# Performance work log

Measured on AMD Instinct MI355X. Metric: run time of the kernel, lower is better.

Reference implementation:

```python
import jax, jax.numpy as jnp
import numpy as np

PRED_STEPS = 12
N_NEG = 100
TEMP = 0.1
EPS = 1e-12


def _l2norm(x):
    # matches torch F.normalize(dim=-1): x / max(||x||, eps)
    n = jnp.sqrt(jnp.sum(x * x, axis=-1, keepdims=True))
    return x / jnp.maximum(n, EPS)


def setup_inputs() -> dict:
    key = jax.random.key(0)
    k1, k2, k3, k4 = jax.random.split(key, 4)
    B, T, D = 8, 256, 256
    context = jax.random.normal(k1, (B, T, D), dtype=jnp.float32)
    targets = jax.random.normal(k2, (B, T, D), dtype=jnp.float32)
    W = jax.random.normal(k3, (PRED_STEPS, D, D), dtype=jnp.float32) * (1.0 / np.sqrt(D))
    b = jax.random.normal(k4, (PRED_STEPS, D), dtype=jnp.float32) * 0.01
    return {"context": context, "targets": targets, "W": W, "b": b}


def reference(context, targets, W, b):
    B, T, D = context.shape
    neg_key = jax.random.key(1234)
    total = jnp.zeros((), dtype=context.dtype)
    count = 0
    for step in range(1, PRED_STEPS + 1):
        if T - step <= 0:
            break
        T2 = T - step
        ctx = context[:, :T2, :]                        # (B,T2,D)
        pos = targets[:, step:, :]                      # (B,T2,D)
        # per-step linear predictor (torch Linear: x @ W^T + b)
        query = jnp.einsum('btd,ed->bte', ctx, W[step - 1]) + b[step - 1]
        query = _l2norm(query)
        pos_n = _l2norm(pos)                            # also serves as the negative pool
        pos_sim = jnp.sum(query * pos_n, axis=-1, keepdims=True) / TEMP  # (B,T2,1)
        # random in-batch negatives (deterministic per-step key)
        neg_idx = jax.random.randint(jax.random.fold_in(neg_key, step),
                                     (B, T2, N_NEG), 0, B * T2)
        flat = pos_n.reshape(B * T2, D)
        negs = flat[neg_idx]                            # (B,T2,K,D) gather
        neg_sim = jnp.einsum('btd,btkd->btk', query, negs) / TEMP  # (B,T2,K)
        logits = jnp.concatenate([pos_sim, neg_sim], axis=-1)      # (B,T2,1+K)
        # cross-entropy with label 0 == -log_softmax(logits)[..., 0], averaged
        loss_step = -jnp.mean(jax.nn.log_softmax(logits, axis=-1)[..., 0])
        total = total + loss_step
        count += 1
    return total / max(count, 1)
```

## Files before the change

kernel.cpp:

```cpp
#include <hip/hip_runtime.h>
#include <stdint.h>

#define BB 8
#define TT 256
#define DD 256
#define NSTEP 12
#define NNEG 100
#define NPART (255 * BB * NSTEP)

typedef _Float16 h2 __attribute__((ext_vector_type(2)));
typedef _Float16 f16x8 __attribute__((ext_vector_type(8)));
typedef float f32x4 __attribute__((ext_vector_type(4)));

#if __has_builtin(__builtin_amdgcn_fdot2)
__device__ __forceinline__ float fdot2(h2 a, h2 b, float c) {
  return __builtin_amdgcn_fdot2(a, b, c, false);
}
#else
__device__ __forceinline__ float fdot2(h2 a, h2 b, float c) {
  return c + (float)a.x * (float)b.x + (float)a.y * (float)b.y;
}
#endif

__device__ __forceinline__ h2 e5m2_lo(uint32_t w) {
#if __has_builtin(__builtin_amdgcn_perm)
  uint32_t r = __builtin_amdgcn_perm(0u, w, 0x010c000cu);
#else
  uint32_t r = ((w & 0xFFu) << 8) | ((w & 0xFF00u) << 16);
#endif
  union { uint32_t u; h2 h; } c; c.u = r; return c.h;
}
__device__ __forceinline__ h2 e5m2_hi(uint32_t w) {
#if __has_builtin(__builtin_amdgcn_perm)
  uint32_t r = __builtin_amdgcn_perm(0u, w, 0x030c020cu);
#else
  uint32_t r = ((w >> 8) & 0xFF00u) | ((w >> 16) & 0xFF000000u) | (((w >> 16) & 0xFFu) << 8);
#endif
  union { uint32_t u; h2 h; } c; c.u = r; return c.h;
}

__device__ __forceinline__ uint32_t f32_to_e5m2(float f) {
  union { _Float16 h; uint16_t u; } c; c.h = (_Float16)f;
  uint16_t h = c.u;
  return (uint32_t)((uint16_t)(h + (uint16_t)0x7F + (uint16_t)((h >> 8) & 1u)) >> 8) & 0xFFu;
}

__host__ __device__ __forceinline__ void tf2x32(uint32_t k0, uint32_t k1,
                                                uint32_t x0, uint32_t x1,
                                                uint32_t &y0, uint32_t &y1) {
  const uint32_t ks2 = k0 ^ k1 ^ 0x1BD11BDAu;
  x0 += k0; x1 += k1;
#define TF_R(r) { x0 += x1; x1 = (x1 << (r)) | (x1 >> (32 - (r))); x1 ^= x0; }
  TF_R(13) TF_R(15) TF_R(26) TF_R(6)
  x0 += k1; x1 += ks2 + 1u;
  TF_R(17) TF_R(29) TF_R(16) TF_R(24)
  x0 += ks2; x1 += k0 + 2u;
  TF_R(13) TF_R(15) TF_R(26) TF_R(6)
  x0 += k0; x1 += k1 + 3u;
  TF_R(17) TF_R(29) TF_R(16) TF_R(24)
  x0 += k1; x1 += ks2 + 4u;
  TF_R(13) TF_R(15) TF_R(26) TF_R(6)
  x0 += ks2; x1 += k0 + 5u;
#undef TF_R
  y0 = x0; y1 = x1;
}

struct IdxParams {
  uint32_t k1x[NSTEP], k1y[NSTEP], k2x[NSTEP], k2y[NSTEP];
  uint32_t mult[NSTEP];
  uint32_t Msp[NSTEP], Ssp[NSTEP], Asp[NSTEP];
  uint32_t Mt2[NSTEP], St2[NSTEP], At2[NSTEP];
};

static void magicu(uint32_t d, uint32_t* M, uint32_t* s, uint32_t* a) {
  uint32_t p, nc, delta, q1, r1, q2, r2;
  *a = 0;
  nc = 0xFFFFFFFFu - (0u - d) % d;
  p = 31;
  q1 = 0x80000000u / nc; r1 = 0x80000000u - q1 * nc;
  q2 = 0x7FFFFFFFu / d;  r2 = 0x7FFFFFFFu - q2 * d;
  do {
    p = p + 1;
    if (r1 >= nc - r1) { q1 = 2*q1 + 1; r1 = 2*r1 - nc; }
    else               { q1 = 2*q1;     r1 = 2*r1; }
    if (r2 + 1 >= d - r2) {
      if (q2 >= 0x7FFFFFFFu) *a = 1;
      q2 = 2*q2 + 1; r2 = 2*r2 + 1 - d;
    } else {
      if (q2 >= 0x80000000u) *a = 1;
      q2 = 2*q2; r2 = 2*r2 + 1;
    }
    delta = d - 1 - r2;
  } while (p < 64 && (q1 < delta || (q1 == delta && r1 == 0)));
  *M = q2 + 1; *s = p - 32;
}

__device__ __forceinline__ uint32_t mdiv(uint32_t n, uint32_t M, uint32_t s, uint32_t a) {
  uint32_t q = __umulhi(n, M);
  if (a) { q = ((n - q) >> 1) + q; return q >> (s - 1); }
  return q >> s;
}

__global__ __launch_bounds__(256) void prep_kernel(const float* __restrict__ tgt,
                                                   const float* __restrict__ ctx,
                                                   const float* __restrict__ W,
                                                   uint8_t* __restrict__ tn8,
                                                   _Float16* __restrict__ ctxh,
                                                   _Float16* __restrict__ Wh) {
  const int bx = blockIdx.x;
  const int tid = threadIdx.x;
  const int lane = tid & 63;
  if (bx < 512) {
    const int row = bx * 4 + (tid >> 6);
    float4 v = ((const float4*)(tgt + (size_t)row * DD))[lane];
    float ss = v.x*v.x + v.y*v.y + v.z*v.z + v.w*v.w;
#pragma unroll
    for (int off = 1; off < 64; off <<= 1) ss += __shfl_xor(ss, off, 64);
    const float sc = 1.0f / fmaxf(sqrtf(ss), 1e-12f);
    const uint32_t p = f32_to_e5m2(v.x * sc) | (f32_to_e5m2(v.y * sc) << 8)
                     | (f32_to_e5m2(v.z * sc) << 16) | (f32_to_e5m2(v.w * sc) << 24);
    ((uint32_t*)(tn8 + (size_t)row * DD))[lane] = p;
  } else {
    union { _Float16 h[4]; uint2 u; } o;
    if (bx < 1024) {
      const int row = (bx - 512) * 4 + (tid >> 6);
      float4 v = ((const float4*)(ctx + (size_t)row * DD))[lane];
      o.h[0] = (_Float16)v.x; o.h[1] = (_Float16)v.y;
      o.h[2] = (_Float16)v.z; o.h[3] = (_Float16)v.w;
      ((uint2*)(ctxh + (size_t)row * DD))[lane] = o.u;
    } else {
      const int row = (bx - 1024) * 4 + (tid >> 6);
      float4 v = ((const float4*)(W + (size_t)row * DD))[lane];
      o.h[0] = (_Float16)v.x; o.h[1] = (_Float16)v.y;
      o.h[2] = (_Float16)v.z; o.h[3] = (_Float16)v.w;
      ((uint2*)(Wh + (size_t)row * DD))[lane] = o.u;
    }
  }
}

__global__ __launch_bounds__(256) void qgemm_mfma_kernel(const _Float16* __restrict__ ctxh,
                                                         const _Float16* __restrict__ Wh,
                                                         const float* __restrict__ bias,
                                                         _Float16* __restrict__ qnh) {
  const int mt  = blockIdx.x;
  const int s   = blockIdx.y;
  const int tid = threadIdx.x;
  const int w   = tid >> 6;
  const int lane = tid & 63;
  const int sl = lane & 15;
  const int q  = lane >> 4;
  const int m0 = mt * 32;

  const _Float16* Arow0 = ctxh + ((size_t)(m0 + sl)) * DD + q * 8;
  const _Float16* Arow1 = Arow0 + (size_t)16 * DD;
  const _Float16* Bbase = Wh + (size_t)s * DD * DD + ((size_t)(w * 64 + sl)) * DD + q * 8;

  f32x4 acc[2][4];
#pragma unroll
  for (int mi = 0; mi < 2; ++mi)
#pragma unroll
    for (int nt = 0; nt < 4; ++nt) acc[mi][nt] = f32x4{0, 0, 0, 0};

#pragma unroll
  for (int k0 = 0; k0 < 8; ++k0) {
    const f16x8 a0 = *(const f16x8*)(Arow0 + k0 * 32);
    const f16x8 a1 = *(const f16x8*)(Arow1 + k0 * 32);
#pragma unroll
    for (int nt = 0; nt < 4; ++nt) {
      const f16x8 b = *(const f16x8*)(Bbase + (size_t)nt * 16 * DD + k0 * 32);
      acc[0][nt] = __builtin_amdgcn_mfma_f32_16x16x32_f16(a0, b, acc[0][nt], 0, 0, 0);
      acc[1][nt] = __builtin_amdgcn_mfma_f32_16x16x32_f16(a1, b, acc[1][nt], 0, 0, 0);
    }
  }
  const float* bp = bias + (size_t)s * DD + w * 64 + sl;
  __shared__ float part[4][32];
#pragma unroll
  for (int mi = 0; mi < 2; ++mi) {
#pragma unroll
    for (int nt = 0; nt < 4; ++nt) {
      const float bv = bp[nt * 16];
#pragma unroll
      for (int r = 0; r < 4; ++r) acc[mi][nt][r] += bv;
    }
    float ss[4];
#pragma unroll
    for (int r = 0; r < 4; ++r) {
      float v = 0.f;
#pragma unroll
      for (int nt = 0; nt < 4; ++nt) v += acc[mi][nt][r] * acc[mi][nt][r];
      ss[r] = v;
    }
#pragma unroll
    for (int off = 1; off < 16; off <<= 1) {
#pragma unroll
      for (int r = 0; r < 4; ++r) ss[r] += __shfl_xor(ss[r], off, 64);
    }
    if (sl == 0) {
#pragma unroll
      for (int r = 0; r < 4; ++r) part[w][mi * 16 + q * 4 + r] = ss[r];
    }
  }
  __syncthreads();
#pragma unroll
  for (int mi = 0; mi < 2; ++mi) {
#pragma unroll
    for (int r = 0; r < 4; ++r) {
      const int row = q * 4 + r;
      const float tot = part[0][mi * 16 + row] + part[1][mi * 16 + row]
                      + part[2][mi * 16 + row] + part[3][mi * 16 + row];
      const float sc = 1.0f / fmaxf(sqrtf(tot), 1e-12f);
      _Float16* outp = qnh + (((size_t)s * (BB * TT)) + m0 + mi * 16 + row) * DD + w * 64 + sl;
#pragma unroll
      for (int nt = 0; nt < 4; ++nt) outp[nt * 16] = (_Float16)(acc[mi][nt][r] * sc);
    }
  }
}

__global__ __launch_bounds__(128) void score_kernel(const IdxParams P,
                                                    const _Float16* __restrict__ qnh,
                                                    const uint8_t* __restrict__ tn8,
                                                    float* __restrict__ partial) {
  const int t    = blockIdx.x;
  const int b    = blockIdx.y;
  const int si   = blockIdx.z;
  const int step = si + 1;
  const int T2   = TT - step;
  const int lin  = (si * BB + b) * 255 + t;
  const int tid  = threadIdx.x;
  if (t >= T2) { if (tid == 0) partial[lin] = 0.f; return; }

  __shared__ int   rowIdx[NNEG + 1];
  __shared__ float logit[NNEG + 1];

  if (tid < NNEG) {
    const uint32_t span = (uint32_t)(BB * T2);
    const uint32_t j = (uint32_t)((b * T2 + t) * NNEG + tid);
    uint32_t h0, h1, l0, l1;
    tf2x32(P.k1x[si], P.k1y[si], 0u, j, h0, h1);
    tf2x32(P.k2x[si], P.k2y[si], 0u, j, l0, l1);
    const uint32_t Msp = P.Msp[si], Ssp = P.Ssp[si], Asp = P.Asp[si];
    const uint32_t hm = h0 - mdiv(h0, Msp, Ssp, Asp) * span;
    const uint32_t lm = l0 - mdiv(l0, Msp, Ssp, Asp) * span;
    const uint32_t off = hm * P.mult[si] + lm;
    const uint32_t om = off - mdiv(off, Msp, Ssp, Asp) * span;
    const uint32_t bb = mdiv(om, P.Mt2[si], P.St2[si], P.At2[si]);
    const uint32_t tt = om - bb * (uint32_t)T2;
    rowIdx[tid + 1] = (int)(bb * TT + tt + (uint32_t)step);
  } else if (tid == NNEG) {
    rowIdx[0] = b * TT + t + step;
  }

  const int g  = tid >> 2;
  const int gl = tid & 3;
  const _Float16* qrow = qnh + (((size_t)si * (BB * TT)) + b * TT + t) * DD;
  uint4 qv[8];
#pragma unroll
  for (int c = 0; c < 4; ++c) {
    qv[c * 2]     = *(const uint4*)(qrow + c * 64 + gl * 16);
    qv[c * 2 + 1] = *(const uint4*)(qrow + c * 64 + gl * 16 + 8);
  }
  __syncthreads();

#pragma unroll
  for (int r = 0; r < 4; ++r) {
    const int k = r * 32 + g;
    if (k <= NNEG) {
      const uint8_t* prow = tn8 + (size_t)rowIdx[k] * DD;
      float d0 = 0.f, d1 = 0.f, d2 = 0.f, d3 = 0.f;
#pragma unroll
      for (int c = 0; c < 4; ++c) {
        const uint4 pv = *(const uint4*)(prow + c * 64 + gl * 16);
        union { uint4 u; h2 h[4]; } qa, qb;
        qa.u = qv[c * 2]; qb.u = qv[c * 2 + 1];
        d0 = fdot2(qa.h[0], e5m2_lo(pv.x), d0);
        d1 = fdot2(qa.h[1], e5m2_hi(pv.x), d1);
        d2 = fdot2(qa.h[2], e5m2_lo(pv.y), d2);
        d3 = fdot2(qa.h[3], e5m2_hi(pv.y), d3);
        d0 = fdot2(qb.h[0], e5m2_lo(pv.z), d0);
        d1 = fdot2(qb.h[1], e5m2_hi(pv.z), d1);
        d2 = fdot2(qb.h[2], e5m2_lo(pv.w), d2);
        d3 = fdot2(qb.h[3], e5m2_hi(pv.w), d3);
      }
      float d = (d0 + d1) + (d2 + d3);
      d += __shfl_xor(d, 1, 64);
      d += __shfl_xor(d, 2, 64);
      if (gl == 0) logit[k] = d * 10.0f;
    }
  }
  __syncthreads();

  if (tid < 64) {
    const int lane = tid;
    const float a = logit[lane];
    const float c = (lane + 64 <= NNEG) ? logit[lane + 64] : -1e30f;
    float m = fmaxf(a, c);
#pragma unroll
    for (int off = 1; off < 64; off <<= 1) m = fmaxf(m, __shfl_xor(m, off, 64));
    float e = __expf(a - m) + ((lane + 64 <= NNEG) ? __expf(c - m) : 0.f);
#pragma unroll
    for (int off = 1; off < 64; off <<= 1) e += __shfl_xor(e, off, 64);
    if (lane == 0) {
      const float lse = m + logf(e);
      partial[lin] = (lse - logit[0]) / (12.0f * (float)(BB * T2));
    }
  }
}

__global__ __launch_bounds__(1024) void final_sum_kernel(const float* __restrict__ partial,
                                                         float* __restrict__ out) {
  __shared__ float wsum[16];
  const int tid = threadIdx.x;
  float s = 0.f;
  const float4* p4 = (const float4*)partial;
  for (int i = tid; i < NPART / 4; i += 1024) {
    const float4 v = p4[i];
    s += v.x + v.y + v.z + v.w;
  }
#pragma unroll
  for (int off = 1; off < 64; off <<= 1) s += __shfl_xor(s, off, 64);
  if ((tid & 63) == 0) wsum[tid >> 6] = s;
  __syncthreads();
  if (tid == 0) {
    float tot = 0.f;
#pragma unroll
    for (int i = 0; i < 16; ++i) tot += wsum[i];
    out[0] = tot;
  }
}

extern "C" void kernel_launch(void* const* d_in, const int* in_sizes, int n_in,
                              void* d_out, int out_size, void* d_ws, size_t ws_size,
                              hipStream_t stream) {
  const float* ctx  = (const float*)d_in[0];
  const float* tgt  = (const float*)d_in[1];
  const float* W    = (const float*)d_in[2];
  const float* bias = (const float*)d_in[3];
  float* out = (float*)d_out;

  uint8_t* tn8   = (uint8_t*)d_ws;
  _Float16* ctxh = (_Float16*)(tn8 + (size_t)BB * TT * DD);
  _Float16* Wh   = ctxh + (size_t)BB * TT * DD;
  _Float16* qnh  = Wh + (size_t)NSTEP * DD * DD;
  float* partial = (float*)(qnh + (size_t)NSTEP * BB * TT * DD);

  IdxParams P;
  for (int s = 0; s < NSTEP; ++s) {
    uint32_t a, b;
    tf2x32(0u, 1234u, 0u, (uint32_t)(s + 1), a, b);
    uint32_t h1a, h1b, h2a, h2b;
    tf2x32(a, b, 0u, 2u, h1a, h1b);
    tf2x32(a, b, 1u, 3u, h2a, h2b);
    P.k1x[s] = h1a; P.k1y[s] = h1b; P.k2x[s] = h2a; P.k2y[s] = h2b;
    const uint32_t T2 = (uint32_t)(TT - (s + 1));
    const uint32_t span = 8u * T2;
    uint32_t m = 65536u % span;
    P.mult[s] = (uint32_t)(((uint64_t)m * m) % span);
    magicu(span, &P.Msp[s], &P.Ssp[s], &P.Asp[s]);
    magicu(T2,   &P.Mt2[s], &P.St2[s], &P.At2[s]);
  }

  hipLaunchKernelGGL(prep_kernel, dim3(1792), dim3(256), 0, stream,
                     tgt, ctx, W, tn8, ctxh, Wh);
  hipLaunchKernelGGL(qgemm_mfma_kernel, dim3(64, NSTEP), dim3(256), 0, stream,
                     ctxh, Wh, bias, qnh);
  hipLaunchKernelGGL(score_kernel, dim3(255, BB, NSTEP), dim3(128), 0, stream,
                     P, qnh, tn8, partial);
  hipLaunchKernelGGL(final_sum_kernel, dim3(1), dim3(1024), 0, stream, partial, out);
}
```

Before: 134.6 us.

## Switch negative scoring to int8 sdot4 and widen the query GEMM to 512 threads

```diff
diff --git a/kernel.cpp b/kernel.cpp
--- a/kernel.cpp
+++ b/kernel.cpp
@@ -12,38 +12,19 @@
 typedef _Float16 f16x8 __attribute__((ext_vector_type(8)));
 typedef float f32x4 __attribute__((ext_vector_type(4)));
 
-#if __has_builtin(__builtin_amdgcn_fdot2)
-__device__ __forceinline__ float fdot2(h2 a, h2 b, float c) {
-  return __builtin_amdgcn_fdot2(a, b, c, false);
+#if __has_builtin(__builtin_amdgcn_sdot4)
+__device__ __forceinline__ int sdot4(uint32_t a, uint32_t b, int c) {
+  return __builtin_amdgcn_sdot4((int)a, (int)b, c, false);
 }
 #else
-__device__ __forceinline__ float fdot2(h2 a, h2 b, float c) {
-  return c + (float)a.x * (float)b.x + (float)a.y * (float)b.y;
+__device__ __forceinline__ int sdot4(uint32_t a, uint32_t b, int c) {
+#pragma unroll
+  for (int i = 0; i < 4; ++i) {
+    c += (int)(int8_t)(a >> (8 * i)) * (int)(int8_t)(b >> (8 * i));
+  }
+  return c;
 }
 #endif
-
-__device__ __forceinline__ h2 e5m2_lo(uint32_t w) {
-#if __has_builtin(__builtin_amdgcn_perm)
-  uint32_t r = __builtin_amdgcn_perm(0u, w, 0x010c000cu);
-#else
-  uint32_t r = ((w & 0xFFu) << 8) | ((w & 0xFF00u) << 16);
-#endif
-  union { uint32_t u; h2 h; } c; c.u = r; return c.h;
-}
-__device__ __forceinline__ h2 e5m2_hi(uint32_t w) {
-#if __has_builtin(__builtin_amdgcn_perm)
-  uint32_t r = __builtin_amdgcn_perm(0u, w, 0x030c020cu);
-#else
-  uint32_t r = ((w >> 8) & 0xFF00u) | ((w >> 16) & 0xFF000000u) | (((w >> 16) & 0xFFu) << 8);
-#endif
-  union { uint32_t u; h2 h; } c; c.u = r; return c.h;
-}
-
-__device__ __forceinline__ uint32_t f32_to_e5m2(float f) {
-  union { _Float16 h; uint16_t u; } c; c.h = (_Float16)f;
-  uint16_t h = c.u;
-  return (uint32_t)((uint16_t)(h + (uint16_t)0x7F + (uint16_t)((h >> 8) & 1u)) >> 8) & 0xFFu;
-}
 
 __host__ __device__ __forceinline__ void tf2x32(uint32_t k0, uint32_t k1,
                                                 uint32_t x0, uint32_t x1,
@@ -101,6 +82,10 @@
   return q >> s;
 }
 
+__device__ __forceinline__ uint32_t q8(float f) {
+  return (uint32_t)(uint8_t)(int8_t)__float2int_rn(127.0f * f);
+}
+
 __global__ __launch_bounds__(256) void prep_kernel(const float* __restrict__ tgt,
                                                    const float* __restrict__ ctx,
                                                    const float* __restrict__ W,
@@ -117,8 +102,8 @@
 #pragma unroll
     for (int off = 1; off < 64; off <<= 1) ss += __shfl_xor(ss, off, 64);
     const float sc = 1.0f / fmaxf(sqrtf(ss), 1e-12f);
-    const uint32_t p = f32_to_e5m2(v.x * sc) | (f32_to_e5m2(v.y * sc) << 8)
-                     | (f32_to_e5m2(v.z * sc) << 16) | (f32_to_e5m2(v.w * sc) << 24);
+    const uint32_t p = q8(v.x * sc) | (q8(v.y * sc) << 8)
+                     | (q8(v.z * sc) << 16) | (q8(v.w * sc) << 24);
     ((uint32_t*)(tn8 + (size_t)row * DD))[lane] = p;
   } else {
     union { _Float16 h[4]; uint2 u; } o;
@@ -138,7 +123,7 @@
   }
 }
 
-__global__ __launch_bounds__(256) void qgemm_mfma_kernel(const _Float16* __restrict__ ctxh,
+__global__ __launch_bounds__(512) void qgemm_mfma_kernel(const _Float16* __restrict__ ctxh,
                                                          const _Float16* __restrict__ Wh,
                                                          const float* __restrict__ bias,
                                                          _Float16* __restrict__ qnh) {
@@ -153,43 +138,39 @@
 
   const _Float16* Arow0 = ctxh + ((size_t)(m0 + sl)) * DD + q * 8;
   const _Float16* Arow1 = Arow0 + (size_t)16 * DD;
-  const _Float16* Bbase = Wh + (size_t)s * DD * DD + ((size_t)(w * 64 + sl)) * DD + q * 8;
-
-  f32x4 acc[2][4];
+  const _Float16* Bbase = Wh + (size_t)s * DD * DD + ((size_t)(w * 32 + sl)) * DD + q * 8;
+
+  f32x4 acc[2][2];
 #pragma unroll
   for (int mi = 0; mi < 2; ++mi)
 #pragma unroll
-    for (int nt = 0; nt < 4; ++nt) acc[mi][nt] = f32x4{0, 0, 0, 0};
+    for (int nt = 0; nt < 2; ++nt) acc[mi][nt] = f32x4{0, 0, 0, 0};
 
 #pragma unroll
   for (int k0 = 0; k0 < 8; ++k0) {
     const f16x8 a0 = *(const f16x8*)(Arow0 + k0 * 32);
     const f16x8 a1 = *(const f16x8*)(Arow1 + k0 * 32);
 #pragma unroll
-    for (int nt = 0; nt < 4; ++nt) {
+    for (int nt = 0; nt < 2; ++nt) {
       const f16x8 b = *(const f16x8*)(Bbase + (size_t)nt * 16 * DD + k0 * 32);
       acc[0][nt] = __builtin_amdgcn_mfma_f32_16x16x32_f16(a0, b, acc[0][nt], 0, 0, 0);
       acc[1][nt] = __builtin_amdgcn_mfma_f32_16x16x32_f16(a1, b, acc[1][nt], 0, 0, 0);
     }
   }
-  const float* bp = bias + (size_t)s * DD + w * 64 + sl;
-  __shared__ float part[4][32];
+  const float* bp = bias + (size_t)s * DD + w * 32 + sl;
+  __shared__ float part[8][32];
 #pragma unroll
   for (int mi = 0; mi < 2; ++mi) {
 #pragma unroll
-    for (int nt = 0; nt < 4; ++nt) {
+    for (int nt = 0; nt < 2; ++nt) {
       const float bv = bp[nt * 16];
 #pragma unroll
       for (int r = 0; r < 4; ++r) acc[mi][nt][r] += bv;
     }
     float ss[4];
 #pragma unroll
-    for (int r = 0; r < 4; ++r) {
-      float v = 0.f;
-#pragma unroll
-      for (int nt = 0; nt < 4; ++nt) v += acc[mi][nt][r] * acc[mi][nt][r];
-      ss[r] = v;
-    }
+    for (int r = 0; r < 4; ++r)
+      ss[r] = acc[mi][0][r] * acc[mi][0][r] + acc[mi][1][r] * acc[mi][1][r];
 #pragma unroll
     for (int off = 1; off < 16; off <<= 1) {
 #pragma unroll
@@ -206,12 +187,13 @@
 #pragma unroll
     for (int r = 0; r < 4; ++r) {
       const int row = q * 4 + r;
-      const float tot = part[0][mi * 16 + row] + part[1][mi * 16 + row]
-                      + part[2][mi * 16 + row] + part[3][mi * 16 + row];
+      float tot = 0.f;
+#pragma unroll
+      for (int wv = 0; wv < 8; ++wv) tot += part[wv][mi * 16 + row];
       const float sc = 1.0f / fmaxf(sqrtf(tot), 1e-12f);
-      _Float16* outp = qnh + (((size_t)s * (BB * TT)) + m0 + mi * 16 + row) * DD + w * 64 + sl;
-#pragma unroll
-      for (int nt = 0; nt < 4; ++nt) outp[nt * 16] = (_Float16)(acc[mi][nt][r] * sc);
+      _Float16* outp = qnh + (((size_t)s * (BB * TT)) + m0 + mi * 16 + row) * DD + w * 32 + sl;
+#pragma unroll
+      for (int nt = 0; nt < 2; ++nt) outp[nt * 16] = (_Float16)(acc[mi][nt][r] * sc);
     }
   }
 }
@@ -253,11 +235,19 @@
   const int g  = tid >> 2;
   const int gl = tid & 3;
   const _Float16* qrow = qnh + (((size_t)si * (BB * TT)) + b * TT + t) * DD;
-  uint4 qv[8];
+  uint32_t qpk[4][4];
 #pragma unroll
   for (int c = 0; c < 4; ++c) {
-    qv[c * 2]     = *(const uint4*)(qrow + c * 64 + gl * 16);
-    qv[c * 2 + 1] = *(const uint4*)(qrow + c * 64 + gl * 16 + 8);
+    union { uint4 u; _Float16 h[8]; } qa, qb;
+    qa.u = *(const uint4*)(qrow + c * 64 + gl * 16);
+    qb.u = *(const uint4*)(qrow + c * 64 + gl * 16 + 8);
+#pragma unroll
+    for (int d = 0; d < 2; ++d) {
+      qpk[c][d]     = q8((float)qa.h[d*4+0]) | (q8((float)qa.h[d*4+1]) << 8)
+                    | (q8((float)qa.h[d*4+2]) << 16) | (q8((float)qa.h[d*4+3]) << 24);
+      qpk[c][d + 2] = q8((float)qb.h[d*4+0]) | (q8((float)qb.h[d*4+1]) << 8)
+                    | (q8((float)qb.h[d*4+2]) << 16) | (q8((float)qb.h[d*4+3]) << 24);
+    }
   }
   __syncthreads();
 
@@ -266,25 +256,18 @@
     const int k = r * 32 + g;
     if (k <= NNEG) {
       const uint8_t* prow = tn8 + (size_t)rowIdx[k] * DD;
-      float d0 = 0.f, d1 = 0.f, d2 = 0.f, d3 = 0.f;
+      int di = 0;
 #pragma unroll
       for (int c = 0; c < 4; ++c) {
         const uint4 pv = *(const uint4*)(prow + c * 64 + gl * 16);
-        union { uint4 u; h2 h[4]; } qa, qb;
-        qa.u = qv[c * 2]; qb.u = qv[c * 2 + 1];
-        d0 = fdot2(qa.h[0], e5m2_lo(pv.x), d0);
-        d1 = fdot2(qa.h[1], e5m2_hi(pv.x), d1);
-        d2 = fdot2(qa.h[2], e5m2_lo(pv.y), d2);
-        d3 = fdot2(qa.h[3], e5m2_hi(pv.y), d3);
-        d0 = fdot2(qb.h[0], e5m2_lo(pv.z), d0);
-        d1 = fdot2(qb.h[1], e5m2_hi(pv.z), d1);
-        d2 = fdot2(qb.h[2], e5m2_lo(pv.w), d2);
-        d3 = fdot2(qb.h[3], e5m2_hi(pv.w), d3);
+        di = sdot4(qpk[c][0], pv.x, di);
+        di = sdot4(qpk[c][1], pv.y, di);
+        di = sdot4(qpk[c][2], pv.z, di);
+        di = sdot4(qpk[c][3], pv.w, di);
       }
-      float d = (d0 + d1) + (d2 + d3);
-      d += __shfl_xor(d, 1, 64);
-      d += __shfl_xor(d, 2, 64);
-      if (gl == 0) logit[k] = d * 10.0f;
+      di += __shfl_xor(di, 1, 64);
+      di += __shfl_xor(di, 2, 64);
+      if (gl == 0) logit[k] = (float)di * (10.0f / 16129.0f);
     }
   }
   __syncthreads();
@@ -361,7 +344,7 @@
 
   hipLaunchKernelGGL(prep_kernel, dim3(1792), dim3(256), 0, stream,
                      tgt, ctx, W, tn8, ctxh, Wh);
-  hipLaunchKernelGGL(qgemm_mfma_kernel, dim3(64, NSTEP), dim3(256), 0, stream,
+  hipLaunchKernelGGL(qgemm_mfma_kernel, dim3(64, NSTEP), dim3(512), 0, stream,
                      ctxh, Wh, bias, qnh);
   hipLaunchKernelGGL(score_kernel, dim3(255, BB, NSTEP), dim3(128), 0, stream,
                      P, qnh, tn8, partial);
```

After: 142.2 us. 1.06x slower.

## Use FP8 MFMA for negative scoring with fp8 queries and targets

Applied to the files above, without the earlier changes.

```diff
diff --git a/kernel.cpp b/kernel.cpp
--- a/kernel.cpp
+++ b/kernel.cpp
@@ -8,42 +8,42 @@
 #define NNEG 100
 #define NPART (255 * BB * NSTEP)
 
-typedef _Float16 h2 __attribute__((ext_vector_type(2)));
+typedef float f32x4 __attribute__((ext_vector_type(4)));
 typedef _Float16 f16x8 __attribute__((ext_vector_type(8)));
-typedef float f32x4 __attribute__((ext_vector_type(4)));
-
-#if __has_builtin(__builtin_amdgcn_fdot2)
-__device__ __forceinline__ float fdot2(h2 a, h2 b, float c) {
-  return __builtin_amdgcn_fdot2(a, b, c, false);
+
+#if __has_builtin(__builtin_amdgcn_cvt_pk_fp8_f32)
+__device__ __forceinline__ uint32_t pk_fp8x4(float x, float y, float z, float w) {
+  int v = 0;
+  v = __builtin_amdgcn_cvt_pk_fp8_f32(x, y, v, false);
+  v = __builtin_amdgcn_cvt_pk_fp8_f32(z, w, v, true);
+  return (uint32_t)v;
+}
+__device__ __forceinline__ uint32_t cvt_fp8(float x) {
+  return (uint32_t)__builtin_amdgcn_cvt_pk_fp8_f32(x, 0.f, 0, false) & 0xFFu;
 }
 #else
-__device__ __forceinline__ float fdot2(h2 a, h2 b, float c) {
-  return c + (float)a.x * (float)b.x + (float)a.y * (float)b.y;
+__device__ __forceinline__ uint32_t cvt_fp8(float f) {
+  union { float f; uint32_t u; } c; c.f = f;
+  uint32_t s = (c.u >> 24) & 0x80u;
+  float a = fabsf(f);
+  if (a > 448.f) return s | 0x7Eu;
+  if (a < 0.001953125f) {
+    uint32_t d = (uint32_t)__float2int_rn(a * 512.0f);
+    return s | d;
+  }
+  int E = 0; float t = a;
+  while (t >= 2.f) { t *= 0.5f; ++E; }
+  while (t < 1.f) { t *= 2.f; --E; }
+  if (E < -6) { uint32_t d = (uint32_t)__float2int_rn(a * 512.0f); return s | d; }
+  uint32_t m = (uint32_t)__float2int_rn((t - 1.f) * 8.f);
+  uint32_t e = (uint32_t)(E + 7);
+  if (m == 8) { m = 0; ++e; }
+  return s | (e << 3) | m;
+}
+__device__ __forceinline__ uint32_t pk_fp8x4(float x, float y, float z, float w) {
+  return cvt_fp8(x) | (cvt_fp8(y) << 8) | (cvt_fp8(z) << 16) | (cvt_fp8(w) << 24);
 }
 #endif
-
-__device__ __forceinline__ h2 e5m2_lo(uint32_t w) {
-#if __has_builtin(__builtin_amdgcn_perm)
-  uint32_t r = __builtin_amdgcn_perm(0u, w, 0x010c000cu);
-#else
-  uint32_t r = ((w & 0xFFu) << 8) | ((w & 0xFF00u) << 16);
-#endif
-  union { uint32_t u; h2 h; } c; c.u = r; return c.h;
-}
-__device__ __forceinline__ h2 e5m2_hi(uint32_t w) {
-#if __has_builtin(__builtin_amdgcn_perm)
-  uint32_t r = __builtin_amdgcn_perm(0u, w, 0x030c020cu);
-#else
-  uint32_t r = ((w >> 8) & 0xFF00u) | ((w >> 16) & 0xFF000000u) | (((w >> 16) & 0xFFu) << 8);
-#endif
-  union { uint32_t u; h2 h; } c; c.u = r; return c.h;
-}
-
-__device__ __forceinline__ uint32_t f32_to_e5m2(float f) {
-  union { _Float16 h; uint16_t u; } c; c.h = (_Float16)f;
-  uint16_t h = c.u;
-  return (uint32_t)((uint16_t)(h + (uint16_t)0x7F + (uint16_t)((h >> 8) & 1u)) >> 8) & 0xFFu;
-}
 
 __host__ __device__ __forceinline__ void tf2x32(uint32_t k0, uint32_t k1,
                                                 uint32_t x0, uint32_t x1,
@@ -117,9 +117,8 @@
 #pragma unroll
     for (int off = 1; off < 64; off <<= 1) ss += __shfl_xor(ss, off, 64);
     const float sc = 1.0f / fmaxf(sqrtf(ss), 1e-12f);
-    const uint32_t p = f32_to_e5m2(v.x * sc) | (f32_to_e5m2(v.y * sc) << 8)
-                     | (f32_to_e5m2(v.z * sc) << 16) | (f32_to_e5m2(v.w * sc) << 24);
-    ((uint32_t*)(tn8 + (size_t)row * DD))[lane] = p;
+    ((uint32_t*)(tn8 + (size_t)row * DD))[lane] =
+        pk_fp8x4(v.x * sc, v.y * sc, v.z * sc, v.w * sc);
   } else {
     union { _Float16 h[4]; uint2 u; } o;
     if (bx < 1024) {
@@ -141,7 +140,7 @@
 __global__ __launch_bounds__(256) void qgemm_mfma_kernel(const _Float16* __restrict__ ctxh,
                                                          const _Float16* __restrict__ Wh,
                                                          const float* __restrict__ bias,
-                                                         _Float16* __restrict__ qnh) {
+                                                         uint8_t* __restrict__ qn8) {
   const int mt  = blockIdx.x;
   const int s   = blockIdx.y;
   const int tid = threadIdx.x;
@@ -209,15 +208,16 @@
       const float tot = part[0][mi * 16 + row] + part[1][mi * 16 + row]
                       + part[2][mi * 16 + row] + part[3][mi * 16 + row];
       const float sc = 1.0f / fmaxf(sqrtf(tot), 1e-12f);
-      _Float16* outp = qnh + (((size_t)s * (BB * TT)) + m0 + mi * 16 + row) * DD + w * 64 + sl;
-#pragma unroll
-      for (int nt = 0; nt < 4; ++nt) outp[nt * 16] = (_Float16)(acc[mi][nt][r] * sc);
+      uint8_t* outp = qn8 + (((size_t)s * (BB * TT)) + m0 + mi * 16 + row) * DD + w * 64 + sl;
+#pragma unroll
+      for (int nt = 0; nt < 4; ++nt)
+        outp[nt * 16] = (uint8_t)cvt_fp8(acc[mi][nt][r] * sc);
     }
   }
 }
 
 __global__ __launch_bounds__(128) void score_kernel(const IdxParams P,
-                                                    const _Float16* __restrict__ qnh,
+                                                    const uint8_t* __restrict__ qn8,
                                                     const uint8_t* __restrict__ tn8,
                                                     float* __restrict__ partial) {
   const int t    = blockIdx.x;
@@ -229,7 +229,7 @@
   const int tid  = threadIdx.x;
   if (t >= T2) { if (tid == 0) partial[lin] = 0.f; return; }
 
-  __shared__ int   rowIdx[NNEG + 1];
+  __shared__ int   rowIdx[112];
   __shared__ float logit[NNEG + 1];
 
   if (tid < NNEG) {
@@ -248,84 +248,70 @@
     rowIdx[tid + 1] = (int)(bb * TT + tt + (uint32_t)step);
   } else if (tid == NNEG) {
     rowIdx[0] = b * TT + t + step;
-  }
-
-  const int g  = tid >> 2;
-  const int gl = tid & 3;
-  const _Float16* qrow = qnh + (((size_t)si * (BB * TT)) + b * TT + t) * DD;
-  uint4 qv[8];
-#pragma unroll
-  for (int c = 0; c < 4; ++c) {
-    qv[c * 2]     = *(const uint4*)(qrow + c * 64 + gl * 16);
-    qv[c * 2 + 1] = *(const uint4*)(qrow + c * 64 + gl * 16 + 8);
-  }
+  } else if (tid < 112) {
+    rowIdx[tid] = 0;
+  }
+
+  const int wv = tid >> 6;
+  const int lane = tid & 63;
+  const int sl = lane & 15;
+  const int qq = lane >> 4;
+  const uint8_t* qrow8 = qn8 + (((size_t)si * (BB * TT)) + b * TT + t) * DD;
+  long bfrag[8];
+#pragma unroll
+  for (int c = 0; c < 8; ++c)
+    bfrag[c] = *(const long*)(qrow8 + c * 32 + qq * 8);
   __syncthreads();
 
-#pragma unroll
-  for (int r = 0; r < 4; ++r) {
-    const int k = r * 32 + g;
-    if (k <= NNEG) {
-      const uint8_t* prow = tn8 + (size_t)rowIdx[k] * DD;
-      float d0 = 0.f, d1 = 0.f, d2 = 0.f, d3 = 0.f;
-#pragma unroll
-      for (int c = 0; c < 4; ++c) {
-        const uint4 pv = *(const uint4*)(prow + c * 64 + gl * 16);
-        union { uint4 u; h2 h[4]; } qa, qb;
-        qa.u = qv[c * 2]; qb.u = qv[c * 2 + 1];
-        d0 = fdot2(qa.h[0], e5m2_lo(pv.x), d0);
-        d1 = fdot2(qa.h[1], e5m2_hi(pv.x), d1);
-        d2 = fdot2(qa.h[2], e5m2_lo(pv.y), d2);
-        d3 = fdot2(qa.h[3], e5m2_hi(pv.y), d3);
-        d0 = fdot2(qb.h[0], e5m2_lo(pv.z), d0);
-        d1 = fdot2(qb.h[1], e5m2_hi(pv.z), d1);
-        d2 = fdot2(qb.h[2], e5m2_lo(pv.w), d2);
-        d3 = fdot2(qb.h[3], e5m2_hi(pv.w), d3);
+  for (int tile = wv; tile < 7; tile += 2) {
+    const uint8_t* pr = tn8 + (size_t)rowIdx[tile * 16 + sl] * DD + qq * 8;
+    f32x4 acc = f32x4{0, 0, 0, 0};
+#pragma unroll
+    for (int c = 0; c < 8; ++c) {
+      const long afrag = *(const long*)(pr + c * 32);
+      acc = __builtin_amdgcn_mfma_f32_16x16x32_fp8_fp8(afrag, bfrag[c], acc, 0, 0, 0);
+    }
+    if (sl == 0) {
+#pragma unroll
+      for (int r = 0; r < 4; ++r) {
+        const int k = tile * 16 + qq * 4 + r;
+        if (k <= NNEG) logit[k] = acc[r] * 10.0f;
       }
-      float d = (d0 + d1) + (d2 + d3);
-      d += __shfl_xor(d, 1, 64);
-      d += __shfl_xor(d, 2, 64);
-      if (gl == 0) logit[k] = d * 10.0f;
     }
   }
   __syncthreads();
 
   if (tid < 64) {
-    const int lane = tid;
-    const float a = logit[lane];
-    const float c = (lane + 64 <= NNEG) ? logit[lane + 64] : -1e30f;
+    const float a = logit[tid];
+    const float c = (tid + 64 <= NNEG) ? logit[tid + 64] : -1e30f;
     float m = fmaxf(a, c);
 #pragma unroll
     for (int off = 1; off < 64; off <<= 1) m = fmaxf(m, __shfl_xor(m, off, 64));
-    float e = __expf(a - m) + ((lane + 64 <= NNEG) ? __expf(c - m) : 0.f);
+    float e = __expf(a - m) + ((tid + 64 <= NNEG) ? __expf(c - m) : 0.f);
 #pragma unroll
     for (int off = 1; off < 64; off <<= 1) e += __shfl_xor(e, off, 64);
-    if (lane == 0) {
+    if (tid == 0) {
       const float lse = m + logf(e);
       partial[lin] = (lse - logit[0]) / (12.0f * (float)(BB * T2));
     }
   }
 }
 
-__global__ __launch_bounds__(1024) void final_sum_kernel(const float* __restrict__ partial,
-                                                         float* __restrict__ out) {
-  __shared__ float wsum[16];
+__global__ __launch_bounds__(256) void final_sum_kernel(const float* __restrict__ partial,
+                                                        float* __restrict__ out) {
+  __shared__ float wsum[4];
   const int tid = threadIdx.x;
+  const int gid = blockIdx.x * 256 + tid;
   float s = 0.f;
-  const float4* p4 = (const float4*)partial;
-  for (int i = tid; i < NPART / 4; i += 1024) {
-    const float4 v = p4[i];
-    s += v.x + v.y + v.z + v.w;
+  if (gid < NPART / 4) {
+    const float4 v = ((const float4*)partial)[gid];
+    s = v.x + v.y + v.z + v.w;
   }
 #pragma unroll
   for (int off = 1; off < 64; off <<= 1) s += __shfl_xor(s, off, 64);
   if ((tid & 63) == 0) wsum[tid >> 6] = s;
   __syncthreads();
-  if (tid == 0) {
-    float tot = 0.f;
-#pragma unroll
-    for (int i = 0; i < 16; ++i) tot += wsum[i];
-    out[0] = tot;
-  }
+  if (tid == 0) atomicAdd(out, wsum[0] + wsum[1] + wsum[2] + wsum[3]);
 }
 
 extern "C" void kernel_launch(void* const* d_in, const int* in_sizes, int n_in,
@@ -340,8 +326,8 @@
   uint8_t* tn8   = (uint8_t*)d_ws;
   _Float16* ctxh = (_Float16*)(tn8 + (size_t)BB * TT * DD);
   _Float16* Wh   = ctxh + (size_t)BB * TT * DD;
-  _Float16* qnh  = Wh + (size_t)NSTEP * DD * DD;
-  float* partial = (float*)(qnh + (size_t)NSTEP * BB * TT * DD);
+  uint8_t* qn8   = (uint8_t*)(Wh + (size_t)NSTEP * DD * DD);
+  float* partial = (float*)(qn8 + (size_t)NSTEP * BB * TT * DD);
 
   IdxParams P;
   for (int s = 0; s < NSTEP; ++s) {
@@ -359,11 +345,13 @@
     magicu(T2,   &P.Mt2[s], &P.St2[s], &P.At2[s]);
   }
 
+  hipMemsetAsync(d_out, 0, sizeof(float), stream);
   hipLaunchKernelGGL(prep_kernel, dim3(1792), dim3(256), 0, stream,
                      tgt, ctx, W, tn8, ctxh, Wh);
   hipLaunchKernelGGL(qgemm_mfma_kernel, dim3(64, NSTEP), dim3(256), 0, stream,
-                     ctxh, Wh, bias, qnh);
+                     ctxh, Wh, bias, qn8);
   hipLaunchKernelGGL(score_kernel, dim3(255, BB, NSTEP), dim3(128), 0, stream,
-                     P, qnh, tn8, partial);
-  hipLaunchKernelGGL(final_sum_kernel, dim3(1), dim3(1024), 0, stream, partial, out);
-}
+                     P, qn8, tn8, partial);
+  hipLaunchKernelGGL(final_sum_kernel, dim3((NPART / 4 + 255) / 256), dim3(256), 0, stream,
+                     partial, out);
+}
```

Result: slower. 237.7 us (+76.6%).

## Fuse prep and q-GEMM with grid barrier; replace final reduction with atomics

Applied to the files above, without the earlier changes.

```diff
diff --git a/kernel.cpp b/kernel.cpp
--- a/kernel.cpp
+++ b/kernel.cpp
@@ -6,7 +6,7 @@
 #define DD 256
 #define NSTEP 12
 #define NNEG 100
-#define NPART (255 * BB * NSTEP)
+#define K1_BLOCKS 768
 
 typedef _Float16 h2 __attribute__((ext_vector_type(2)));
 typedef _Float16 f16x8 __attribute__((ext_vector_type(8)));
@@ -101,52 +101,61 @@
   return q >> s;
 }
 
-__global__ __launch_bounds__(256) void prep_kernel(const float* __restrict__ tgt,
-                                                   const float* __restrict__ ctx,
-                                                   const float* __restrict__ W,
-                                                   uint8_t* __restrict__ tn8,
-                                                   _Float16* __restrict__ ctxh,
-                                                   _Float16* __restrict__ Wh) {
-  const int bx = blockIdx.x;
-  const int tid = threadIdx.x;
+__global__ __launch_bounds__(256, 3) void k1_prep_qgemm(const float* __restrict__ tgt,
+                                                        const float* __restrict__ ctx,
+                                                        const float* __restrict__ W,
+                                                        const float* __restrict__ bias,
+                                                        uint8_t* __restrict__ tn8,
+                                                        _Float16* __restrict__ ctxh,
+                                                        _Float16* __restrict__ Wh,
+                                                        _Float16* __restrict__ qnh,
+                                                        uint32_t* __restrict__ barrier_cnt) {
+  const int bx   = blockIdx.x;
+  const int tid  = threadIdx.x;
   const int lane = tid & 63;
-  if (bx < 512) {
-    const int row = bx * 4 + (tid >> 6);
-    float4 v = ((const float4*)(tgt + (size_t)row * DD))[lane];
-    float ss = v.x*v.x + v.y*v.y + v.z*v.z + v.w*v.w;
-#pragma unroll
-    for (int off = 1; off < 64; off <<= 1) ss += __shfl_xor(ss, off, 64);
-    const float sc = 1.0f / fmaxf(sqrtf(ss), 1e-12f);
-    const uint32_t p = f32_to_e5m2(v.x * sc) | (f32_to_e5m2(v.y * sc) << 8)
-                     | (f32_to_e5m2(v.z * sc) << 16) | (f32_to_e5m2(v.w * sc) << 24);
-    ((uint32_t*)(tn8 + (size_t)row * DD))[lane] = p;
-  } else {
-    union { _Float16 h[4]; uint2 u; } o;
-    if (bx < 1024) {
-      const int row = (bx - 512) * 4 + (tid >> 6);
-      float4 v = ((const float4*)(ctx + (size_t)row * DD))[lane];
-      o.h[0] = (_Float16)v.x; o.h[1] = (_Float16)v.y;
-      o.h[2] = (_Float16)v.z; o.h[3] = (_Float16)v.w;
-      ((uint2*)(ctxh + (size_t)row * DD))[lane] = o.u;
+
+  const int gw = bx * 4 + (tid >> 6);
+  for (int task = gw; task < 7168; task += 3072) {
+    if (task < 2048) {
+      float4 v = ((const float4*)(tgt + (size_t)task * DD))[lane];
+      float ss = v.x*v.x + v.y*v.y + v.z*v.z + v.w*v.w;
+#pragma unroll
+      for (int off = 1; off < 64; off <<= 1) ss += __shfl_xor(ss, off, 64);
+      const float sc = 1.0f / fmaxf(sqrtf(ss), 1e-12f);
+      const uint32_t p = f32_to_e5m2(v.x * sc) | (f32_to_e5m2(v.y * sc) << 8)
+                       | (f32_to_e5m2(v.z * sc) << 16) | (f32_to_e5m2(v.w * sc) << 24);
+      ((uint32_t*)(tn8 + (size_t)task * DD))[lane] = p;
     } else {
-      const int row = (bx - 1024) * 4 + (tid >> 6);
-      float4 v = ((const float4*)(W + (size_t)row * DD))[lane];
-      o.h[0] = (_Float16)v.x; o.h[1] = (_Float16)v.y;
-      o.h[2] = (_Float16)v.z; o.h[3] = (_Float16)v.w;
-      ((uint2*)(Wh + (size_t)row * DD))[lane] = o.u;
-    }
-  }
-}
-
-__global__ __launch_bounds__(256) void qgemm_mfma_kernel(const _Float16* __restrict__ ctxh,
-                                                         const _Float16* __restrict__ Wh,
-                                                         const float* __restrict__ bias,
-                                                         _Float16* __restrict__ qnh) {
-  const int mt  = blockIdx.x;
-  const int s   = blockIdx.y;
-  const int tid = threadIdx.x;
-  const int w   = tid >> 6;
-  const int lane = tid & 63;
+      union { _Float16 h[4]; uint2 u; } o;
+      if (task < 4096) {
+        const int row = task - 2048;
+        float4 v = ((const float4*)(ctx + (size_t)row * DD))[lane];
+        o.h[0] = (_Float16)v.x; o.h[1] = (_Float16)v.y;
+        o.h[2] = (_Float16)v.z; o.h[3] = (_Float16)v.w;
+        ((uint2*)(ctxh + (size_t)row * DD))[lane] = o.u;
+      } else {
+        const int row = task - 4096;
+        float4 v = ((const float4*)(W + (size_t)row * DD))[lane];
+        o.h[0] = (_Float16)v.x; o.h[1] = (_Float16)v.y;
+        o.h[2] = (_Float16)v.z; o.h[3] = (_Float16)v.w;
+        ((uint2*)(Wh + (size_t)row * DD))[lane] = o.u;
+      }
+    }
+  }
+
+  __syncthreads();
+  if (tid == 0) {
+    __threadfence();
+    atomicAdd(barrier_cnt, 1u);
+    while (atomicAdd(barrier_cnt, 0u) < (uint32_t)K1_BLOCKS)
+      __builtin_amdgcn_s_sleep(2);
+    __threadfence();
+  }
+  __syncthreads();
+
+  const int mt = bx & 63;
+  const int s  = bx >> 6;
+  const int w  = tid >> 6;
   const int sl = lane & 15;
   const int q  = lane >> 4;
   const int m0 = mt * 32;
@@ -219,15 +228,14 @@
 __global__ __launch_bounds__(128) void score_kernel(const IdxParams P,
                                                     const _Float16* __restrict__ qnh,
                                                     const uint8_t* __restrict__ tn8,
-                                                    float* __restrict__ partial) {
+                                                    float* __restrict__ out) {
   const int t    = blockIdx.x;
   const int b    = blockIdx.y;
   const int si   = blockIdx.z;
   const int step = si + 1;
   const int T2   = TT - step;
-  const int lin  = (si * BB + b) * 255 + t;
   const int tid  = threadIdx.x;
-  if (t >= T2) { if (tid == 0) partial[lin] = 0.f; return; }
+  if (t >= T2) return;
 
   __shared__ int   rowIdx[NNEG + 1];
   __shared__ float logit[NNEG + 1];
@@ -290,41 +298,18 @@
   __syncthreads();
 
   if (tid < 64) {
-    const int lane = tid;
-    const float a = logit[lane];
-    const float c = (lane + 64 <= NNEG) ? logit[lane + 64] : -1e30f;
+    const float a = logit[tid];
+    const float c = (tid + 64 <= NNEG) ? logit[tid + 64] : -1e30f;
     float m = fmaxf(a, c);
 #pragma unroll
     for (int off = 1; off < 64; off <<= 1) m = fmaxf(m, __shfl_xor(m, off, 64));
-    float e = __expf(a - m) + ((lane + 64 <= NNEG) ? __expf(c - m) : 0.f);
+    float e = __expf(a - m) + ((tid + 64 <= NNEG) ? __expf(c - m) : 0.f);
 #pragma unroll
     for (int off = 1; off < 64; off <<= 1) e += __shfl_xor(e, off, 64);
-    if (lane == 0) {
+    if (tid == 0) {
       const float lse = m + logf(e);
-      partial[lin] = (lse - logit[0]) / (12.0f * (float)(BB * T2));
-    }
-  }
-}
-
-__global__ __launch_bounds__(1024) void final_sum_kernel(const float* __restrict__ partial,
-                                                         float* __restrict__ out) {
-  __shared__ float wsum[16];
-  const int tid = threadIdx.x;
-  float s = 0.f;
-  const float4* p4 = (const float4*)partial;
-  for (int i = tid; i < NPART / 4; i += 1024) {
-    const float4 v = p4[i];
-    s += v.x + v.y + v.z + v.w;
-  }
-#pragma unroll
-  for (int off = 1; off < 64; off <<= 1) s += __shfl_xor(s, off, 64);
-  if ((tid & 63) == 0) wsum[tid >> 6] = s;
-  __syncthreads();
-  if (tid == 0) {
-    float tot = 0.f;
-#pragma unroll
-    for (int i = 0; i < 16; ++i) tot += wsum[i];
-    out[0] = tot;
+      atomicAdd(out, (lse - logit[0]) / (12.0f * (float)(BB * T2)));
+    }
   }
 }
 
@@ -341,7 +326,7 @@
   _Float16* ctxh = (_Float16*)(tn8 + (size_t)BB * TT * DD);
   _Float16* Wh   = ctxh + (size_t)BB * TT * DD;
   _Float16* qnh  = Wh + (size_t)NSTEP * DD * DD;
-  float* partial = (float*)(qnh + (size_t)NSTEP * BB * TT * DD);
+  uint32_t* cnt  = (uint32_t*)(qnh + (size_t)NSTEP * BB * TT * DD);
 
   IdxParams P;
   for (int s = 0; s < NSTEP; ++s) {
@@ -359,11 +344,10 @@
     magicu(T2,   &P.Mt2[s], &P.St2[s], &P.At2[s]);
   }
 
-  hipLaunchKernelGGL(prep_kernel, dim3(1792), dim3(256), 0, stream,
-                     tgt, ctx, W, tn8, ctxh, Wh);
-  hipLaunchKernelGGL(qgemm_mfma_kernel, dim3(64, NSTEP), dim3(256), 0, stream,
-                     ctxh, Wh, bias, qnh);
+  hipMemsetAsync(out, 0, sizeof(float), stream);
+  hipMemsetAsync(cnt, 0, sizeof(uint32_t), stream);
+  hipLaunchKernelGGL(k1_prep_qgemm, dim3(K1_BLOCKS), dim3(256), 0, stream,
+                     tgt, ctx, W, bias, tn8, ctxh, Wh, qnh, cnt);
   hipLaunchKernelGGL(score_kernel, dim3(255, BB, NSTEP), dim3(128), 0, stream,
-                     P, qnh, tn8, partial);
-  hipLaunchKernelGGL(final_sum_kernel, dim3(1), dim3(1024), 0, stream, partial, out);
-}
+                     P, qnh, tn8, out);
+}
```

After: 473.3 us. 3.52x slower.
